# Optimization experiments

Measured on AMD Instinct MI355X. Metric: run time of the kernel, lower is better.

The kernel has to match this reference:

```python
import jax, jax.numpy as jnp
import numpy as np

# Module hyperparameters (init_kwargs)
THRESHOLD_ABS = 0.2
THRESHOLD_REL = 0.05   # set to None to disable the relative-threshold branch
MIN_DISTANCE = 3


def setup_inputs() -> dict:
    key = jax.random.key(0)
    # belief maps in [0, 1), NCHW
    belive_map = jax.random.uniform(key, (32, 4, 512, 512), dtype=jnp.float32)
    return {"belive_map": belive_map}


def reference(belive_map):
    """Peak detection on belief maps (dense, jit-friendly form).

    Faithful to BeliveMapsNMS.forward: the torch module additionally compacts
    the mask into (coords, labels, scores) lists via nonzero/gather, which has
    data-dependent shapes; here we return the equivalent dense outputs:
      mask        [B,C,H,W] bool   - peak locations (nonzero of this == torch ind)
      scores_abs  [B,C,H,W] f32    - belief value at peaks, 0 elsewhere
      scores_rel  [B,C,H,W] f32    - scores_abs / per-(b,c) max
    """
    k = 2 * MIN_DISTANCE + 1          # 7
    pad = k // 2                       # 3 -> 'same' max pool, stride 1

    # F.max_pool2d(kernel=k, stride=1, padding=k//2)
    x_max = jax.lax.reduce_window(
        belive_map, -jnp.inf, jax.lax.max,
        window_dimensions=(1, 1, k, k),
        window_strides=(1, 1, 1, 1),
        padding=[(0, 0), (0, 0), (pad, pad), (pad, pad)],
    )

    # per-(batch, channel) global max: hh.max(dim=2) on the flattened map
    vmax = jnp.max(belive_map, axis=(2, 3), keepdims=True)  # [B,C,1,1]

    mask = (x_max == belive_map) & (belive_map > THRESHOLD_ABS)
    if THRESHOLD_REL is not None:
        mask = mask & (belive_map > THRESHOLD_REL * vmax)

    scores_abs = jnp.where(mask, belive_map, jnp.float32(0.0))
    scores_rel = scores_abs / vmax
    return mask, scores_abs, scores_rel
```

## Files before the change

### kernel.cpp

```cpp
#include <hip/hip_runtime.h>
#include <math.h>


#define H 512
#define W 512
#define PLANE_ELEMS (H * W)
#define TX 64
#define TY 64
#define HALO 3
#define SIN_STRIDE 72
#define SROW_STRIDE 68
#define OFF 1

__global__ __launch_bounds__(256) void vmax_kernel(const float* __restrict__ in,
                                                   unsigned int* __restrict__ vmax_bits) {
    const int q = blockIdx.x;
    const int plane = blockIdx.y;
    const float4* p = (const float4*)(in + (size_t)plane * PLANE_ELEMS + q * (PLANE_ELEMS / 4));
    float m = 0.0f;
    const int nvec = PLANE_ELEMS / 4 / 4;
    for (int i = threadIdx.x; i < nvec; i += 256) {
        float4 v = p[i];
        m = fmaxf(m, fmaxf(fmaxf(v.x, v.y), fmaxf(v.z, v.w)));
    }
    #pragma unroll
    for (int o = 32; o > 0; o >>= 1) m = fmaxf(m, __shfl_down(m, o, 64));
    __shared__ float s[4];
    const int wid = threadIdx.x >> 6;
    const int lane = threadIdx.x & 63;
    if (lane == 0) s[wid] = m;
    __syncthreads();
    if (threadIdx.x == 0) {
        m = fmaxf(fmaxf(s[0], s[1]), fmaxf(s[2], s[3]));
        atomicMax(&vmax_bits[plane], __float_as_uint(m));
    }
}

__global__ __launch_bounds__(256) void nms_kernel(const float* __restrict__ in,
                                                  const unsigned int* __restrict__ vmax_bits,
                                                  float* __restrict__ out, int N) {
    const int plane = blockIdx.y;
    const int tile = blockIdx.x;
    const int tx0 = (tile & 7) * TX;
    const int ty0 = (tile >> 3) * TY;
    const float* pin = in + (size_t)plane * PLANE_ELEMS;

    __shared__ __align__(16) float sIn[(TY + 6) * SIN_STRIDE];
    __shared__ __align__(16) float sRow[(TY + 6) * SROW_STRIDE];

    for (int i = threadIdx.x; i < (TY + 6) * (TX + 6); i += 256) {
        const int y = i / (TX + 6);
        const int x = i - y * (TX + 6);
        const int gy = ty0 + y - HALO;
        const int gx = tx0 + x - HALO;
        float v = -INFINITY;
        if (gy >= 0 && gy < H && gx >= 0 && gx < W) v = pin[gy * W + gx];
        sIn[y * SIN_STRIDE + OFF + x] = v;
    }
    __syncthreads();

    for (int i = threadIdx.x; i < (TY + 6) * TX; i += 256) {
        const int y = i >> 6;
        const int x = i & (TX - 1);
        const float* r = &sIn[y * SIN_STRIDE + OFF + x];
        float m = r[0];
        m = fmaxf(m, r[1]); m = fmaxf(m, r[2]); m = fmaxf(m, r[3]);
        m = fmaxf(m, r[4]); m = fmaxf(m, r[5]); m = fmaxf(m, r[6]);
        sRow[y * SROW_STRIDE + x] = m;
    }
    __syncthreads();

    const float vmax = __uint_as_float(vmax_bits[plane]);
    const float rel_thr = 0.05f * vmax;
    const float inv_vmax = 1.0f / vmax;

    float* __restrict__ omask = out;
    float* __restrict__ oabs = out + (size_t)N;
    float* __restrict__ orel = out + 2 * (size_t)N;
    const size_t outBase = (size_t)plane * PLANE_ELEMS;

    for (int i = threadIdx.x; i < TY * (TX / 4); i += 256) {
        const int y = i >> 4;
        const int xg = i & 15;
        const int x = xg * 4;
        const float* c = &sRow[y * SROW_STRIDE + x];
        float4 m = *(const float4*)c;
        #pragma unroll
        for (int dy = 1; dy < 7; ++dy) {
            float4 v = *(const float4*)(c + dy * SROW_STRIDE);
            m.x = fmaxf(m.x, v.x); m.y = fmaxf(m.y, v.y);
            m.z = fmaxf(m.z, v.z); m.w = fmaxf(m.w, v.w);
        }
        const float4 ctr = *(const float4*)&sIn[(y + HALO) * SIN_STRIDE + OFF + HALO + x];

        float4 msk, ab, rl;
        {
            const bool p0 = (m.x == ctr.x) & (ctr.x > 0.2f) & (ctr.x > rel_thr);
            const bool p1 = (m.y == ctr.y) & (ctr.y > 0.2f) & (ctr.y > rel_thr);
            const bool p2 = (m.z == ctr.z) & (ctr.z > 0.2f) & (ctr.z > rel_thr);
            const bool p3 = (m.w == ctr.w) & (ctr.w > 0.2f) & (ctr.w > rel_thr);
            msk.x = p0 ? 1.0f : 0.0f; ab.x = p0 ? ctr.x : 0.0f; rl.x = ab.x * inv_vmax;
            msk.y = p1 ? 1.0f : 0.0f; ab.y = p1 ? ctr.y : 0.0f; rl.y = ab.y * inv_vmax;
            msk.z = p2 ? 1.0f : 0.0f; ab.z = p2 ? ctr.z : 0.0f; rl.z = ab.z * inv_vmax;
            msk.w = p3 ? 1.0f : 0.0f; ab.w = p3 ? ctr.w : 0.0f; rl.w = ab.w * inv_vmax;
        }
        const size_t o = outBase + (size_t)(ty0 + y) * W + (tx0 + x);
        *(float4*)(omask + o) = msk;
        *(float4*)(oabs + o) = ab;
        *(float4*)(orel + o) = rl;
    }
}

extern "C" void kernel_launch(void* const* d_in, const int* in_sizes, int n_in,
                              void* d_out, int out_size, void* d_ws, size_t ws_size,
                              hipStream_t stream) {
    const float* in = (const float*)d_in[0];
    float* out = (float*)d_out;
    const int N = in_sizes[0];
    const int planes = N / PLANE_ELEMS;

    unsigned int* vmax_bits = (unsigned int*)d_ws;
    hipMemsetAsync(vmax_bits, 0, planes * sizeof(unsigned int), stream);

    vmax_kernel<<<dim3(4, planes), 256, 0, stream>>>(in, vmax_bits);
    nms_kernel<<<dim3((H / TX) * (W / TY), planes), 256, 0, stream>>>(in, vmax_bits, out, N);
}
```

Measured before the change: 572.4 us.

## Use full-width row strips with shuffle-based horizontal max and nontemporal stores

Tiles change from 64x64 to full-width 16-row strips, so the horizontal halo disappears and each row is read with vectorized float4 loads. The horizontal 7-wide max is computed in registers using wave shuffles and prefix/suffix maxima instead of a staged shared-memory pass. The vertical max reuses suffix maxima across 8 output rows per thread, and the center value is re-read from global memory. Outputs use nontemporal stores to avoid polluting the cache. The shared buffer grows to about 45KB, which may limit occupancy, and the vertical halo overhead rises to 22/16.

```diff
diff --git a/kernel.cpp b/kernel.cpp
--- a/kernel.cpp
+++ b/kernel.cpp
@@ -5,12 +5,20 @@
 #define H 512
 #define W 512
 #define PLANE_ELEMS (H * W)
-#define TX 64
-#define TY 64
-#define HALO 3
-#define SIN_STRIDE 72
-#define SROW_STRIDE 68
-#define OFF 1
+#define TH 16
+#define LROWS (TH + 6)
+#define NEG_INF (-INFINITY)
+
+typedef float v4f __attribute__((ext_vector_type(4)));
+
+__device__ __forceinline__ float4 vmax4(float4 a, float4 b) {
+    return make_float4(fmaxf(a.x, b.x), fmaxf(a.y, b.y), fmaxf(a.z, b.z), fmaxf(a.w, b.w));
+}
+
+__device__ __forceinline__ void nt_store4(float* p, float a, float b, float c, float d) {
+    v4f v = {a, b, c, d};
+    __builtin_nontemporal_store(v, (v4f*)p);
+}
 
 __global__ __launch_bounds__(256) void vmax_kernel(const float* __restrict__ in,
                                                    unsigned int* __restrict__ vmax_bits) {
@@ -26,9 +34,7 @@
     #pragma unroll
     for (int o = 32; o > 0; o >>= 1) m = fmaxf(m, __shfl_down(m, o, 64));
     __shared__ float s[4];
-    const int wid = threadIdx.x >> 6;
-    const int lane = threadIdx.x & 63;
-    if (lane == 0) s[wid] = m;
+    if ((threadIdx.x & 63) == 0) s[threadIdx.x >> 6] = m;
     __syncthreads();
     if (threadIdx.x == 0) {
         m = fmaxf(fmaxf(s[0], s[1]), fmaxf(s[2], s[3]));
@@ -40,33 +46,45 @@
                                                   const unsigned int* __restrict__ vmax_bits,
                                                   float* __restrict__ out, int N) {
     const int plane = blockIdx.y;
-    const int tile = blockIdx.x;
-    const int tx0 = (tile & 7) * TX;
-    const int ty0 = (tile >> 3) * TY;
+    const int ty0 = blockIdx.x * TH;
     const float* pin = in + (size_t)plane * PLANE_ELEMS;
 
-    __shared__ __align__(16) float sIn[(TY + 6) * SIN_STRIDE];
-    __shared__ __align__(16) float sRow[(TY + 6) * SROW_STRIDE];
+    __shared__ __align__(16) float sRow[LROWS * W];
 
-    for (int i = threadIdx.x; i < (TY + 6) * (TX + 6); i += 256) {
-        const int y = i / (TX + 6);
-        const int x = i - y * (TX + 6);
-        const int gy = ty0 + y - HALO;
-        const int gx = tx0 + x - HALO;
-        float v = -INFINITY;
-        if (gy >= 0 && gy < H && gx >= 0 && gx < W) v = pin[gy * W + gx];
-        sIn[y * SIN_STRIDE + OFF + x] = v;
-    }
-    __syncthreads();
+    const int wid = threadIdx.x >> 6;
+    const int lane = threadIdx.x & 63;
+    const int c8 = lane << 3;
 
-    for (int i = threadIdx.x; i < (TY + 6) * TX; i += 256) {
-        const int y = i >> 6;
-        const int x = i & (TX - 1);
-        const float* r = &sIn[y * SIN_STRIDE + OFF + x];
-        float m = r[0];
-        m = fmaxf(m, r[1]); m = fmaxf(m, r[2]); m = fmaxf(m, r[3]);
-        m = fmaxf(m, r[4]); m = fmaxf(m, r[5]); m = fmaxf(m, r[6]);
-        sRow[y * SROW_STRIDE + x] = m;
+    for (int r = wid; r < LROWS; r += 4) {
+        const int gy = ty0 + r - 3;
+        float4 v0, v1;
+        if (gy >= 0 && gy < H) {
+            const float4* row = (const float4*)(pin + (size_t)gy * W);
+            v0 = row[lane * 2];
+            v1 = row[lane * 2 + 1];
+        } else {
+            v0 = v1 = make_float4(NEG_INF, NEG_INF, NEG_INF, NEG_INF);
+        }
+        float l0 = __shfl_up(v1.y, 1, 64), l1 = __shfl_up(v1.z, 1, 64), l2 = __shfl_up(v1.w, 1, 64);
+        float r0 = __shfl_down(v0.x, 1, 64), r1 = __shfl_down(v0.y, 1, 64), r2 = __shfl_down(v0.z, 1, 64);
+        if (lane == 0) { l0 = NEG_INF; l1 = NEG_INF; l2 = NEG_INF; }
+        if (lane == 63) { r0 = NEG_INF; r1 = NEG_INF; r2 = NEG_INF; }
+        float a[14] = {l0, l1, l2, v0.x, v0.y, v0.z, v0.w, v1.x, v1.y, v1.z, v1.w, r0, r1, r2};
+        float A[7];
+        A[6] = a[6];
+        #pragma unroll
+        for (int j = 5; j >= 0; --j) A[j] = fmaxf(a[j], A[j + 1]);
+        float rm[8];
+        rm[0] = A[0];
+        float B = a[7];
+        rm[1] = fmaxf(A[1], B);
+        #pragma unroll
+        for (int j = 2; j <= 6; ++j) { B = fmaxf(B, a[6 + j]); rm[j] = fmaxf(A[j], B); }
+        B = fmaxf(B, a[13]);
+        rm[7] = B;
+        float4* dst = (float4*)&sRow[r * W + c8];
+        dst[0] = make_float4(rm[0], rm[1], rm[2], rm[3]);
+        dst[1] = make_float4(rm[4], rm[5], rm[6], rm[7]);
     }
     __syncthreads();
 
@@ -77,37 +95,44 @@
     float* __restrict__ omask = out;
     float* __restrict__ oabs = out + (size_t)N;
     float* __restrict__ orel = out + 2 * (size_t)N;
-    const size_t outBase = (size_t)plane * PLANE_ELEMS;
 
-    for (int i = threadIdx.x; i < TY * (TX / 4); i += 256) {
-        const int y = i >> 4;
-        const int xg = i & 15;
-        const int x = xg * 4;
-        const float* c = &sRow[y * SROW_STRIDE + x];
-        float4 m = *(const float4*)c;
-        #pragma unroll
-        for (int dy = 1; dy < 7; ++dy) {
-            float4 v = *(const float4*)(c + dy * SROW_STRIDE);
-            m.x = fmaxf(m.x, v.x); m.y = fmaxf(m.y, v.y);
-            m.z = fmaxf(m.z, v.z); m.w = fmaxf(m.w, v.w);
+    const int strip = threadIdx.x >> 7;
+    const int cg = threadIdx.x & 127;
+    const int c = cg << 2;
+    const int y0 = strip << 3;
+
+    float4 Lr[7], Aq[7];
+    #pragma unroll
+    for (int k = 0; k < 7; ++k) Lr[k] = *(const float4*)&sRow[(y0 + k) * W + c];
+    Aq[6] = Lr[6];
+    #pragma unroll
+    for (int j = 5; j >= 0; --j) Aq[j] = vmax4(Lr[j], Aq[j + 1]);
+
+    const int gy_base = ty0 + y0;
+    float4 Bq;
+    #pragma unroll
+    for (int i = 0; i < 8; ++i) {
+        float4 m;
+        if (i == 0) {
+            m = Aq[0];
+        } else {
+            float4 row = *(const float4*)&sRow[(y0 + 6 + i) * W + c];
+            Bq = (i == 1) ? row : vmax4(Bq, row);
+            m = (i == 7) ? Bq : vmax4(Aq[i], Bq);
         }
-        const float4 ctr = *(const float4*)&sIn[(y + HALO) * SIN_STRIDE + OFF + HALO + x];
-
-        float4 msk, ab, rl;
-        {
-            const bool p0 = (m.x == ctr.x) & (ctr.x > 0.2f) & (ctr.x > rel_thr);
-            const bool p1 = (m.y == ctr.y) & (ctr.y > 0.2f) & (ctr.y > rel_thr);
-            const bool p2 = (m.z == ctr.z) & (ctr.z > 0.2f) & (ctr.z > rel_thr);
-            const bool p3 = (m.w == ctr.w) & (ctr.w > 0.2f) & (ctr.w > rel_thr);
-            msk.x = p0 ? 1.0f : 0.0f; ab.x = p0 ? ctr.x : 0.0f; rl.x = ab.x * inv_vmax;
-            msk.y = p1 ? 1.0f : 0.0f; ab.y = p1 ? ctr.y : 0.0f; rl.y = ab.y * inv_vmax;
-            msk.z = p2 ? 1.0f : 0.0f; ab.z = p2 ? ctr.z : 0.0f; rl.z = ab.z * inv_vmax;
-            msk.w = p3 ? 1.0f : 0.0f; ab.w = p3 ? ctr.w : 0.0f; rl.w = ab.w * inv_vmax;
-        }
-        const size_t o = outBase + (size_t)(ty0 + y) * W + (tx0 + x);
-        *(float4*)(omask + o) = msk;
-        *(float4*)(oabs + o) = ab;
-        *(float4*)(orel + o) = rl;
+        const int gy = gy_base + i;
+        const float4 ctr = *(const float4*)(pin + (size_t)gy * W + c);
+        const bool p0 = (m.x == ctr.x) & (ctr.x > 0.2f) & (ctr.x > rel_thr);
+        const bool p1 = (m.y == ctr.y) & (ctr.y > 0.2f) & (ctr.y > rel_thr);
+        const bool p2 = (m.z == ctr.z) & (ctr.z > 0.2f) & (ctr.z > rel_thr);
+        const bool p3 = (m.w == ctr.w) & (ctr.w > 0.2f) & (ctr.w > rel_thr);
+        const float a0 = p0 ? ctr.x : 0.0f, a1 = p1 ? ctr.y : 0.0f;
+        const float a2 = p2 ? ctr.z : 0.0f, a3 = p3 ? ctr.w : 0.0f;
+        const size_t o = (size_t)plane * PLANE_ELEMS + (size_t)gy * W + c;
+        nt_store4(omask + o, p0 ? 1.0f : 0.0f, p1 ? 1.0f : 0.0f,
+                             p2 ? 1.0f : 0.0f, p3 ? 1.0f : 0.0f);
+        nt_store4(oabs + o, a0, a1, a2, a3);
+        nt_store4(orel + o, a0 * inv_vmax, a1 * inv_vmax, a2 * inv_vmax, a3 * inv_vmax);
     }
 }
 
@@ -120,8 +145,8 @@
     const int planes = N / PLANE_ELEMS;
 
     unsigned int* vmax_bits = (unsigned int*)d_ws;
-    hipMemsetAsync(vmax_bits, 0, planes * sizeof(unsigned int), stream);
+    (void)hipMemsetAsync(vmax_bits, 0, planes * sizeof(unsigned int), stream);
 
     vmax_kernel<<<dim3(4, planes), 256, 0, stream>>>(in, vmax_bits);
-    nms_kernel<<<dim3((H / TX) * (W / TY), planes), 256, 0, stream>>>(in, vmax_bits, out, N);
+    nms_kernel<<<dim3(H / TH, planes), 256, 0, stream>>>(in, vmax_bits, out, N);
 }
```

After: 492.9 us. 1.16x faster.
